# Kernel tuning notes

Hardware: AMD Instinct MI355X
Metric: run time of the kernel (lower is better)

The kernel has to match this reference:

```python
import jax, jax.numpy as jnp
import numpy as np

B, H, S, D = 4, 16, 2048, 128

def setup_inputs() -> dict:
    key = jax.random.key(0)
    k1, k2 = jax.random.split(key)
    x2 = jax.random.normal(k1, (B, H, S, D), dtype=jnp.float32)
    x3 = jax.random.normal(k2, (B, H, S, D), dtype=jnp.float32)
    return {"x2": x2, "x3": x3}

def reference(x2, x3):
    # scores: [B,H,S,S] = x2 @ x3^T (unscaled)
    scores = jnp.einsum('bhqd,bhkd->bhqk', x2, x3)
    probs = jax.nn.softmax(scores, axis=-1)
    # output: [B,H,S,D] = probs @ x3
    return jnp.einsum('bhqk,bhkd->bhqd', probs, x3)
```

## Files before the change

kernel.cpp:

```cpp
#include <hip/hip_runtime.h>
#include <hip/hip_bf16.h>

typedef __attribute__((ext_vector_type(4))) float f32x4;
typedef _Float16 f16;
typedef __attribute__((ext_vector_type(8))) _Float16 f16x8;
typedef __attribute__((ext_vector_type(4))) _Float16 f16x4;
typedef __attribute__((ext_vector_type(2))) __fp16 pk16x2;

#define S_LEN 2048
#define D_DIM 128
#define QBLK 128
#define KVBLK 64
#define NKV (S_LEN / KVBLK)

__global__ __launch_bounds__(256, 2) void attn_kernel(
    const float* __restrict__ Q, const float* __restrict__ KV,
    float* __restrict__ Out)
{
    unsigned b = blockIdx.x;
    unsigned cpx = gridDim.x >> 3;
    unsigned work = (b & 7u) * cpx + (b >> 3);
    unsigned head = work >> 4;
    unsigned qt = work & 15u;

    const float* Qh = Q + (size_t)head * (S_LEN * D_DIM) + (size_t)qt * QBLK * D_DIM;
    const float* Kh = KV + (size_t)head * (S_LEN * D_DIM);
    float* Oh = Out + (size_t)head * (S_LEN * D_DIM) + (size_t)qt * QBLK * D_DIM;

    const int tid = threadIdx.x;
    const int wv = tid >> 6;
    const int lane = tid & 63;
    const int lo = lane & 15;
    const int hi = lane >> 4;

    __shared__ __align__(16) f16 Ksh[KVBLK * D_DIM];
    __shared__ __align__(16) f16 Vsh[D_DIM * KVBLK];
    __shared__ __align__(16) f16 Psh[4][2][16 * KVBLK];

    const int srow = (tid >> 5) * 8;
    const int scol = (tid & 31) * 4;

    f16x8 qf[2][4];
    #pragma unroll
    for (int t = 0; t < 2; ++t) {
        const float* qr = Qh + (wv * 32 + t * 16 + lo) * D_DIM + hi * 8;
        #pragma unroll
        for (int kc = 0; kc < 4; ++kc) {
            f32x4 a = *(const f32x4*)(qr + kc * 32);
            f32x4 c = *(const f32x4*)(qr + kc * 32 + 4);
            pk16x2 p0 = __builtin_amdgcn_cvt_pkrtz(a[0], a[1]);
            pk16x2 p1 = __builtin_amdgcn_cvt_pkrtz(a[2], a[3]);
            pk16x2 p2 = __builtin_amdgcn_cvt_pkrtz(c[0], c[1]);
            pk16x2 p3 = __builtin_amdgcn_cvt_pkrtz(c[2], c[3]);
            f16x8 q;
            q[0] = (f16)p0[0]; q[1] = (f16)p0[1]; q[2] = (f16)p1[0]; q[3] = (f16)p1[1];
            q[4] = (f16)p2[0]; q[5] = (f16)p2[1]; q[6] = (f16)p3[0]; q[7] = (f16)p3[1];
            qf[t][kc] = q;
        }
    }

    f32x4 oacc[2][8];
    #pragma unroll
    for (int t = 0; t < 2; ++t)
        #pragma unroll
        for (int n = 0; n < 8; ++n) oacc[t][n] = (f32x4){0.f, 0.f, 0.f, 0.f};
    float mr[2] = {-1e30f, -1e30f};
    float lr[2] = {0.f, 0.f};

    f32x4 stg[8];

    #define STAGE_LOAD(KT) do {                                               \
        const float* p_ = Kh + (size_t)(KT) * KVBLK * D_DIM + srow * D_DIM + scol; \
        _Pragma("unroll")                                                     \
        for (int i_ = 0; i_ < 8; ++i_) stg[i_] = *(const f32x4*)(p_ + i_ * D_DIM); \
    } while (0)

    #define STAGE_WRITE() do {                                                \
        _Pragma("unroll")                                                     \
        for (int i_ = 0; i_ < 8; ++i_) {                                      \
            int row_ = srow + i_;                                             \
            int fK_ = (row_ & 7) ^ ((row_ >> 3) & 7);                         \
            pk16x2 a_ = __builtin_amdgcn_cvt_pkrtz(stg[i_][0], stg[i_][1]);   \
            pk16x2 b_ = __builtin_amdgcn_cvt_pkrtz(stg[i_][2], stg[i_][3]);   \
            f16x4 w_;                                                         \
            w_[0] = (f16)a_[0]; w_[1] = (f16)a_[1];                           \
            w_[2] = (f16)b_[0]; w_[3] = (f16)b_[1];                           \
            *(f16x4*)&Ksh[row_ * D_DIM + (scol ^ (fK_ << 3))] = w_;           \
        }                                                                     \
        _Pragma("unroll")                                                     \
        for (int j_ = 0; j_ < 4; ++j_) {                                      \
            int d_ = scol + j_;                                               \
            int g_ = (d_ & 7) ^ ((d_ >> 3) & 7);                              \
            pk16x2 a0_ = __builtin_amdgcn_cvt_pkrtz(stg[0][j_], stg[1][j_]);  \
            pk16x2 a1_ = __builtin_amdgcn_cvt_pkrtz(stg[2][j_], stg[3][j_]);  \
            pk16x2 a2_ = __builtin_amdgcn_cvt_pkrtz(stg[4][j_], stg[5][j_]);  \
            pk16x2 a3_ = __builtin_amdgcn_cvt_pkrtz(stg[6][j_], stg[7][j_]);  \
            f16x8 w_;                                                         \
            w_[0] = (f16)a0_[0]; w_[1] = (f16)a0_[1];                         \
            w_[2] = (f16)a1_[0]; w_[3] = (f16)a1_[1];                         \
            w_[4] = (f16)a2_[0]; w_[5] = (f16)a2_[1];                         \
            w_[6] = (f16)a3_[0]; w_[7] = (f16)a3_[1];                         \
            *(f16x8*)&Vsh[d_ * KVBLK + (srow ^ (g_ << 3))] = w_;              \
        }                                                                     \
    } while (0)

    STAGE_LOAD(0);
    STAGE_WRITE();
    __syncthreads();

    for (int kt = 0; kt < NKV; ++kt) {
        if (kt + 1 < NKV) STAGE_LOAD(kt + 1);

        f32x4 st[2][4];
        #pragma unroll
        for (int t = 0; t < 2; ++t)
            #pragma unroll
            for (int m = 0; m < 4; ++m) st[t][m] = (f32x4){0.f, 0.f, 0.f, 0.f};
        __builtin_amdgcn_s_setprio(1);
        #pragma unroll
        for (int m = 0; m < 4; ++m) {
            int row = m * 16 + lo;
            int fK = (row & 7) ^ ((row >> 3) & 7);
            #pragma unroll
            for (int kc = 0; kc < 4; ++kc) {
                f16x8 kf = *(const f16x8*)&Ksh[row * D_DIM + ((kc * 32 + hi * 8) ^ (fK << 3))];
                st[0][m] = __builtin_amdgcn_mfma_f32_16x16x32_f16(kf, qf[0][kc], st[0][m], 0, 0, 0);
                st[1][m] = __builtin_amdgcn_mfma_f32_16x16x32_f16(kf, qf[1][kc], st[1][m], 0, 0, 0);
            }
        }
        __builtin_amdgcn_s_setprio(0);

        const int swp = (lo & 7) << 3;
        #pragma unroll
        for (int t = 0; t < 2; ++t) {
            float tmax = -1e30f;
            #pragma unroll
            for (int m = 0; m < 4; ++m)
                #pragma unroll
                for (int r = 0; r < 4; ++r) tmax = fmaxf(tmax, st[t][m][r]);
            tmax = fmaxf(tmax, __shfl_xor(tmax, 16, 64));
            tmax = fmaxf(tmax, __shfl_xor(tmax, 32, 64));

            bool skip = __all(tmax - mr[t] <= 8.0f);
            float mnew = skip ? mr[t] : fmaxf(mr[t], tmax);

            float ls = 0.f;
            #pragma unroll
            for (int m = 0; m < 4; ++m) {
                #pragma unroll
                for (int r = 0; r < 4; ++r) {
                    float p = __expf(st[t][m][r] - mnew);
                    st[t][m][r] = p;
                    ls += p;
                }
            }
            ls += __shfl_xor(ls, 16, 64);
            ls += __shfl_xor(ls, 32, 64);

            if (!skip) {
                float scale = __expf(mr[t] - mnew);
                lr[t] = lr[t] * scale + ls;
                float sc4[4];
                #pragma unroll
                for (int r = 0; r < 4; ++r) sc4[r] = __shfl(scale, hi * 4 + r, 64);
                #pragma unroll
                for (int n = 0; n < 8; ++n)
                    #pragma unroll
                    for (int r = 0; r < 4; ++r) oacc[t][n][r] *= sc4[r];
                mr[t] = mnew;
            } else {
                lr[t] += ls;
            }

            #pragma unroll
            for (int m = 0; m < 4; ++m) {
                pk16x2 a2 = __builtin_amdgcn_cvt_pkrtz(st[t][m][0], st[t][m][1]);
                pk16x2 b2 = __builtin_amdgcn_cvt_pkrtz(st[t][m][2], st[t][m][3]);
                f16x4 w;
                w[0] = (f16)a2[0]; w[1] = (f16)a2[1]; w[2] = (f16)b2[0]; w[3] = (f16)b2[1];
                int col = (m * 16 + hi * 4) ^ swp;
                *(f16x4*)&Psh[wv][t][lo * KVBLK + col] = w;
            }
        }

        __builtin_amdgcn_s_setprio(1);
        #pragma unroll
        for (int kc2 = 0; kc2 < 2; ++kc2) {
            f16x8 pf0 = *(const f16x8*)&Psh[wv][0][lo * KVBLK + ((kc2 * 32 + hi * 8) ^ swp)];
            f16x8 pf1 = *(const f16x8*)&Psh[wv][1][lo * KVBLK + ((kc2 * 32 + hi * 8) ^ swp)];
            #pragma unroll
            for (int n = 0; n < 8; ++n) {
                int d = n * 16 + lo;
                int g = (d & 7) ^ ((d >> 3) & 7);
                f16x8 vf = *(const f16x8*)&Vsh[d * KVBLK + ((kc2 * 32 + hi * 8) ^ (g << 3))];
                oacc[0][n] = __builtin_amdgcn_mfma_f32_16x16x32_f16(pf0, vf, oacc[0][n], 0, 0, 0);
                oacc[1][n] = __builtin_amdgcn_mfma_f32_16x16x32_f16(pf1, vf, oacc[1][n], 0, 0, 0);
            }
        }
        __builtin_amdgcn_s_setprio(0);

        __syncthreads();
        if (kt + 1 < NKV) {
            STAGE_WRITE();
            __syncthreads();
        }
    }

    #pragma unroll
    for (int t = 0; t < 2; ++t) {
        float inv = 1.0f / lr[t];
        float rl[4];
        #pragma unroll
        for (int r = 0; r < 4; ++r) rl[r] = __shfl(inv, hi * 4 + r, 64);
        #pragma unroll
        for (int n = 0; n < 8; ++n)
            #pragma unroll
            for (int r = 0; r < 4; ++r)
                Oh[(wv * 32 + t * 16 + hi * 4 + r) * D_DIM + n * 16 + lo] = oacc[t][n][r] * rl[r];
    }
}

extern "C" void kernel_launch(void* const* d_in, const int* in_sizes, int n_in,
                              void* d_out, int out_size, void* d_ws, size_t ws_size,
                              hipStream_t stream) {
    const float* x2 = (const float*)d_in[0];
    const float* x3 = (const float*)d_in[1];
    float* out = (float*)d_out;
    dim3 grid(1024), block(256);
    hipLaunchKernelGGL(attn_kernel, grid, block, 0, stream, x2, x3, out);
}
```

Baseline: 175.3 us.

## Remap softmax probabilities into MFMA operands via permlane swaps instead of LDS

Converts the P tile from the QK^T MFMA accumulator layout to the A-operand layout of the PV MFMA in registers, using permlane32_swap and permlane16_swap. This removes the per-wave Psh shared buffer along with its writes and reads. The cross-lane row max and row sum reductions also move from __shfl_xor (ds_bpermute) to permlane swaps. The aim is to cut LDS traffic and latency in the inner loop and free shared memory, at the cost of extra VALU permute instructions and reliance on getting the lane mapping exactly right.

```diff
diff --git a/kernel.cpp b/kernel.cpp
--- a/kernel.cpp
+++ b/kernel.cpp
@@ -6,12 +6,26 @@
 typedef __attribute__((ext_vector_type(8))) _Float16 f16x8;
 typedef __attribute__((ext_vector_type(4))) _Float16 f16x4;
 typedef __attribute__((ext_vector_type(2))) __fp16 pk16x2;
+typedef __attribute__((ext_vector_type(2))) unsigned int uint2v;
 
 #define S_LEN 2048
 #define D_DIM 128
 #define QBLK 128
 #define KVBLK 64
 #define NKV (S_LEN / KVBLK)
+
+__device__ __forceinline__ float hired_max(float x) {
+    uint2v s = __builtin_amdgcn_permlane16_swap(__float_as_uint(x), __float_as_uint(x), false, false);
+    float m = fmaxf(__uint_as_float(s.x), __uint_as_float(s.y));
+    uint2v s2 = __builtin_amdgcn_permlane32_swap(__float_as_uint(m), __float_as_uint(m), false, false);
+    return fmaxf(__uint_as_float(s2.x), __uint_as_float(s2.y));
+}
+__device__ __forceinline__ float hired_sum(float x) {
+    uint2v s = __builtin_amdgcn_permlane16_swap(__float_as_uint(x), __float_as_uint(x), false, false);
+    float m = __uint_as_float(s.x) + __uint_as_float(s.y);
+    uint2v s2 = __builtin_amdgcn_permlane32_swap(__float_as_uint(m), __float_as_uint(m), false, false);
+    return __uint_as_float(s2.x) + __uint_as_float(s2.y);
+}
 
 __global__ __launch_bounds__(256, 2) void attn_kernel(
     const float* __restrict__ Q, const float* __restrict__ KV,
@@ -35,7 +49,6 @@
 
     __shared__ __align__(16) f16 Ksh[KVBLK * D_DIM];
     __shared__ __align__(16) f16 Vsh[D_DIM * KVBLK];
-    __shared__ __align__(16) f16 Psh[4][2][16 * KVBLK];
 
     const int srow = (tid >> 5) * 8;
     const int scol = (tid & 31) * 4;
@@ -130,7 +143,7 @@
         }
         __builtin_amdgcn_s_setprio(0);
 
-        const int swp = (lo & 7) << 3;
+        f16x8 pf[2][2];
         #pragma unroll
         for (int t = 0; t < 2; ++t) {
             float tmax = -1e30f;
@@ -138,8 +151,7 @@
             for (int m = 0; m < 4; ++m)
                 #pragma unroll
                 for (int r = 0; r < 4; ++r) tmax = fmaxf(tmax, st[t][m][r]);
-            tmax = fmaxf(tmax, __shfl_xor(tmax, 16, 64));
-            tmax = fmaxf(tmax, __shfl_xor(tmax, 32, 64));
+            tmax = hired_max(tmax);
 
             bool skip = __all(tmax - mr[t] <= 8.0f);
             float mnew = skip ? mr[t] : fmaxf(mr[t], tmax);
@@ -154,8 +166,7 @@
                     ls += p;
                 }
             }
-            ls += __shfl_xor(ls, 16, 64);
-            ls += __shfl_xor(ls, 32, 64);
+            ls = hired_sum(ls);
 
             if (!skip) {
                 float scale = __expf(mr[t] - mnew);
@@ -172,29 +183,38 @@
                 lr[t] += ls;
             }
 
+            unsigned cc[4][2];
             #pragma unroll
             for (int m = 0; m < 4; ++m) {
-                pk16x2 a2 = __builtin_amdgcn_cvt_pkrtz(st[t][m][0], st[t][m][1]);
-                pk16x2 b2 = __builtin_amdgcn_cvt_pkrtz(st[t][m][2], st[t][m][3]);
-                f16x4 w;
-                w[0] = (f16)a2[0]; w[1] = (f16)a2[1]; w[2] = (f16)b2[0]; w[3] = (f16)b2[1];
-                int col = (m * 16 + hi * 4) ^ swp;
-                *(f16x4*)&Psh[wv][t][lo * KVBLK + col] = w;
+                union { pk16x2 p; unsigned u; } ua, ub;
+                ua.p = __builtin_amdgcn_cvt_pkrtz(st[t][m][0], st[t][m][1]);
+                ub.p = __builtin_amdgcn_cvt_pkrtz(st[t][m][2], st[t][m][3]);
+                cc[m][0] = ua.u; cc[m][1] = ub.u;
+            }
+            #pragma unroll
+            for (int kc2 = 0; kc2 < 2; ++kc2) {
+                unsigned r0 = cc[2 * kc2][0], r1 = cc[2 * kc2][1];
+                unsigned r2 = cc[2 * kc2 + 1][0], r3 = cc[2 * kc2 + 1][1];
+                uint2v s02 = __builtin_amdgcn_permlane32_swap(r0, r2, false, false);
+                uint2v s13 = __builtin_amdgcn_permlane32_swap(r1, r3, false, false);
+                uint2v t02 = __builtin_amdgcn_permlane16_swap(s02.x, s02.y, false, false);
+                uint2v t13 = __builtin_amdgcn_permlane16_swap(s13.x, s13.y, false, false);
+                union { unsigned u[4]; f16x8 v; } pu;
+                pu.u[0] = t02.x; pu.u[1] = t13.x; pu.u[2] = t02.y; pu.u[3] = t13.y;
+                pf[t][kc2] = pu.v;
             }
         }
 
         __builtin_amdgcn_s_setprio(1);
         #pragma unroll
         for (int kc2 = 0; kc2 < 2; ++kc2) {
-            f16x8 pf0 = *(const f16x8*)&Psh[wv][0][lo * KVBLK + ((kc2 * 32 + hi * 8) ^ swp)];
-            f16x8 pf1 = *(const f16x8*)&Psh[wv][1][lo * KVBLK + ((kc2 * 32 + hi * 8) ^ swp)];
             #pragma unroll
             for (int n = 0; n < 8; ++n) {
                 int d = n * 16 + lo;
                 int g = (d & 7) ^ ((d >> 3) & 7);
                 f16x8 vf = *(const f16x8*)&Vsh[d * KVBLK + ((kc2 * 32 + hi * 8) ^ (g << 3))];
-                oacc[0][n] = __builtin_amdgcn_mfma_f32_16x16x32_f16(pf0, vf, oacc[0][n], 0, 0, 0);
-                oacc[1][n] = __builtin_amdgcn_mfma_f32_16x16x32_f16(pf1, vf, oacc[1][n], 0, 0, 0);
+                oacc[0][n] = __builtin_amdgcn_mfma_f32_16x16x32_f16(pf[0][kc2], vf, oacc[0][n], 0, 0, 0);
+                oacc[1][n] = __builtin_amdgcn_mfma_f32_16x16x32_f16(pf[1][kc2], vf, oacc[1][n], 0, 0, 0);
             }
         }
         __builtin_amdgcn_s_setprio(0);
```

Result: faster. 170.0 us (-3.1%).
